# Optimization experiments

Hardware: AMD Instinct MI355X
Metric: run time of the kernel (lower is better)

Reference implementation:

```python
import jax, jax.numpy as jnp
import numpy as np

D_MODEL = 1024
NUM_HEADS = 16
D_K = D_MODEL // NUM_HEADS
THETA = 10000.0


def _apply_rope(x, positions):
    # x: [B, H, S, d_k], positions: [B, S]
    dk = x.shape[-1]
    freq = 1.0 / (THETA ** (jnp.arange(0, dk, 2, dtype=jnp.float32) / dk))  # [dk/2]
    ang = positions.astype(jnp.float32)[:, None, :, None] * freq  # [B,1,S,dk/2]
    cos, sin = jnp.cos(ang), jnp.sin(ang)
    x_even = x[..., 0::2]
    x_odd = x[..., 1::2]
    re = x_even * cos - x_odd * sin
    ro = x_even * sin + x_odd * cos
    # interleave back: [..., dk/2, 2] -> [..., dk]
    return jnp.stack([re, ro], axis=-1).reshape(x.shape)


def setup_inputs() -> dict:
    key = jax.random.key(0)
    kx, kq, kk, kv, ko = jax.random.split(key, 5)
    B, S = 2, 2048
    std = (2.0 / (D_MODEL + D_MODEL)) ** 0.5
    x = jax.random.normal(kx, (B, S, D_MODEL), dtype=jnp.float32)
    Wq = jax.random.normal(kq, (D_MODEL, D_MODEL), dtype=jnp.float32) * std
    Wk = jax.random.normal(kk, (D_MODEL, D_MODEL), dtype=jnp.float32) * std
    Wv = jax.random.normal(kv, (D_MODEL, D_MODEL), dtype=jnp.float32) * std
    Wo = jax.random.normal(ko, (D_MODEL, D_MODEL), dtype=jnp.float32) * std
    token_positions = jnp.tile(jnp.arange(S, dtype=jnp.int32)[None, :], (B, 1))
    return {"x": x, "Wq": Wq, "Wk": Wk, "Wv": Wv, "Wo": Wo,
            "token_positions": token_positions}


def reference(x, Wq, Wk, Wv, Wo, token_positions):
    B, S, D = x.shape
    H, dk = NUM_HEADS, D_K
    scale = 1.0 / np.sqrt(dk)
    # Linear is y = x @ W.T with W:[d_out, d_in]
    q = jnp.einsum('bsd,ed->bse', x, Wq).reshape(B, S, H, dk).transpose(0, 2, 1, 3)
    k = jnp.einsum('bsd,ed->bse', x, Wk).reshape(B, S, H, dk).transpose(0, 2, 1, 3)
    v = jnp.einsum('bsd,ed->bse', x, Wv).reshape(B, S, H, dk).transpose(0, 2, 1, 3)
    q = _apply_rope(q, token_positions)
    k = _apply_rope(k, token_positions)
    scores = jnp.einsum('bhqd,bhkd->bhqk', q, k) * scale  # [B,H,S,S]
    causal = jnp.tril(jnp.ones((S, S), dtype=bool))
    scores = jnp.where(causal[None, None, :, :], scores, -jnp.inf)
    probs = jax.nn.softmax(scores, axis=-1)
    attn = jnp.einsum('bhqk,bhkd->bhqd', probs, v)  # [B,H,S,dk]
    attn = attn.transpose(0, 2, 1, 3).reshape(B, S, D)
    return jnp.einsum('bsd,ed->bse', attn, Wo)
```

## Files before the change

### kernel.cpp

```cpp
#include <hip/hip_runtime.h>
#include <hip/hip_bf16.h>
#include <math.h>

#define B_  2
#define S_  2048
#define H_  16
#define D_  1024
#define DK_ 64

typedef __attribute__((ext_vector_type(8))) short bf16x8;
typedef __attribute__((ext_vector_type(8))) unsigned short ushort8v;
typedef __attribute__((ext_vector_type(4))) float f32x4;

__device__ __forceinline__ unsigned short f2bf(float f) {
  unsigned u = __float_as_uint(f);
  unsigned r = (u + 0x7FFFu + ((u >> 16) & 1u)) >> 16;
  return (unsigned short)r;
}
__device__ __forceinline__ unsigned pack_trunc(float lo, float hi) {
  return (__float_as_uint(lo) >> 16) | (__float_as_uint(hi) & 0xffff0000u);
}
__device__ __forceinline__ float fast_exp2(float x) {
#if __has_builtin(__builtin_amdgcn_exp2f)
  return __builtin_amdgcn_exp2f(x);
#else
  return __expf(x * 0.69314718056f);
#endif
}
__device__ __forceinline__ void gload_lds16(const unsigned short* g,
                                            unsigned short* l) {
  __builtin_amdgcn_global_load_lds(
      (const __attribute__((address_space(1))) unsigned int*)(const void*)g,
      (__attribute__((address_space(3))) unsigned int*)(void*)l, 16, 0, 0);
}

__global__ __launch_bounds__(256)
void cast5_bf16(const float* __restrict__ x,  const float* __restrict__ wq,
                const float* __restrict__ wk, const float* __restrict__ wv,
                const float* __restrict__ wo,
                unsigned short* __restrict__ xb,  unsigned short* __restrict__ wqb,
                unsigned short* __restrict__ wkb, unsigned short* __restrict__ wvb,
                unsigned short* __restrict__ wob)
{
  const int idx = blockIdx.x;
  const float* s; unsigned short* d; int lblk;
  if (idx < 2048) { s = x; d = xb; lblk = idx; }
  else {
    int t = idx - 2048;
    int w = t >> 9;
    lblk  = t & 511;
    s = (w == 0) ? wq  : (w == 1) ? wk  : (w == 2) ? wv  : wo;
    d = (w == 0) ? wqb : (w == 1) ? wkb : (w == 2) ? wvb : wob;
  }
  size_t i0 = ((size_t)lblk * 256 + threadIdx.x) * 8;
  float4 v0 = *(const float4*)(s + i0);
  float4 v1 = *(const float4*)(s + i0 + 4);
  ushort8v o;
  o[0] = f2bf(v0.x); o[1] = f2bf(v0.y); o[2] = f2bf(v0.z); o[3] = f2bf(v0.w);
  o[4] = f2bf(v1.x); o[5] = f2bf(v1.y); o[6] = f2bf(v1.z); o[7] = f2bf(v1.w);
  *(ushort8v*)(d + i0) = o;
}

__global__ __launch_bounds__(256)
void gemm_qkv(const unsigned short* __restrict__ A0,
              const unsigned short* __restrict__ W0,
              const unsigned short* __restrict__ W1,
              const unsigned short* __restrict__ W2,
              unsigned short* __restrict__ qh,
              unsigned short* __restrict__ kh,
              unsigned short* __restrict__ vt,
              const int* __restrict__ tp)
{
  const int z = blockIdx.z;

  __shared__ unsigned short As[128 * 64];
  __shared__ unsigned short Bs[128 * 64];
  __shared__ int tps[128];

  const int tid   = threadIdx.x;
  const int wave  = tid >> 6;
  const int lane  = tid & 63;
  const int quad  = lane >> 4;
  const int col16 = lane & 15;
  const int wr    = (wave >> 1) * 64;
  const int wc    = (wave & 1) * 64;

  const int row0 = (z == 2) ? blockIdx.x * 128 : blockIdx.y * 128;
  const int col0 = (z == 2) ? blockIdx.y * 128 : blockIdx.x * 128;
  const unsigned short* Aptr = (z == 2) ? W2 : A0;
  const unsigned short* Bptr = (z == 0) ? W0 : (z == 1) ? W1 : A0;

  if (z < 2 && tid < 128) tps[tid] = tp[row0 + tid];

  const int srow = wave * 8 + (lane >> 3);
  const int scol = ((lane & 7) ^ ((lane >> 3) & 7)) * 8;
  const unsigned short* gA = Aptr + (size_t)(row0 + srow) * D_ + scol;
  const unsigned short* gB = Bptr + (size_t)(col0 + srow) * D_ + scol;

  f32x4 acc[4][4];
  #pragma unroll
  for (int mt = 0; mt < 4; ++mt)
    #pragma unroll
    for (int nt = 0; nt < 4; ++nt)
      #pragma unroll
      for (int r = 0; r < 4; ++r) acc[mt][nt][r] = 0.f;

  for (int k0 = 0; k0 < D_; k0 += 64) {
    __syncthreads();
    #pragma unroll
    for (int p = 0; p < 4; ++p) {
      gload_lds16(gA + (size_t)(p * 32) * D_ + k0, &As[(p * 32 + wave * 8) * 64]);
      gload_lds16(gB + (size_t)(p * 32) * D_ + k0, &Bs[(p * 32 + wave * 8) * 64]);
    }
    __syncthreads();

    #pragma unroll
    for (int h = 0; h < 2; ++h) {
      const int jo = ((h * 4 + quad) ^ (col16 & 7)) * 8;
      bf16x8 af[4], bfr[4];
      #pragma unroll
      for (int mt = 0; mt < 4; ++mt)
        af[mt] = *(const bf16x8*)&As[(wr + mt * 16 + col16) * 64 + jo];
      #pragma unroll
      for (int nt = 0; nt < 4; ++nt)
        bfr[nt] = *(const bf16x8*)&Bs[(wc + nt * 16 + col16) * 64 + jo];

      #pragma unroll
      for (int mt = 0; mt < 4; ++mt)
        #pragma unroll
        for (int nt = 0; nt < 4; ++nt)
          acc[mt][nt] = __builtin_amdgcn_mfma_f32_16x16x32_bf16(
              af[mt], bfr[nt], acc[mt][nt], 0, 0, 0);
    }
  }

  if (z == 2) {
    #pragma unroll
    for (int mt = 0; mt < 4; ++mt)
      #pragma unroll
      for (int r = 0; r < 4; ++r) {
        int c = row0 + wr + mt * 16 + quad * 4 + r;
        int h = c >> 6, d = c & 63;
        #pragma unroll
        for (int nt = 0; nt < 4; ++nt) {
          int t  = col0 + wc + nt * 16 + col16;
          int bb = t >> 11, sl = t & (S_ - 1);
          vt[((size_t)((bb << 4) + h) * DK_ + d) * S_ + sl] =
              f2bf(acc[mt][nt][r]);
        }
      }
  } else {
    unsigned short* C = z ? kh : qh;
    const float qs = z ? 1.0f : 0.1803368801111204f;
    const float sgn = (col16 & 1) ? 1.f : -1.f;
    float freqr[4];
    #pragma unroll
    for (int nt = 0; nt < 4; ++nt) {
      int i = ((wc + nt * 16 + col16) & 63) >> 1;
      freqr[nt] = exp2f(-0.4152410118f * (float)i);
    }
    #pragma unroll
    for (int mt = 0; mt < 4; ++mt)
      #pragma unroll
      for (int r = 0; r < 4; ++r) {
        int rl  = wr + mt * 16 + quad * 4 + r;
        int row = row0 + rl;
        float p = (float)tps[rl];
        #pragma unroll
        for (int nt = 0; nt < 4; ++nt) {
          int col = col0 + wc + nt * 16 + col16;
          float ang = p * freqr[nt];
          float sn = __sinf(ang), cs = __cosf(ang);
          float val = acc[mt][nt][r];
          float oth = __shfl_xor(val, 1);
          C[(size_t)row * D_ + col] = f2bf((val * cs + oth * sgn * sn) * qs);
        }
      }
  }
}

__global__ __launch_bounds__(256)
void gemm_wo(const unsigned short* __restrict__ A,
             const unsigned short* __restrict__ W,
             float* __restrict__ C)
{
  __shared__ unsigned short As[64 * 64];
  __shared__ unsigned short Bs[128 * 64];

  const int tid   = threadIdx.x;
  const int wave  = tid >> 6;
  const int lane  = tid & 63;
  const int quad  = lane >> 4;
  const int col16 = lane & 15;
  const int row0  = blockIdx.y * 64;
  const int col0  = blockIdx.x * 128;
  const int wr    = (wave >> 1) * 32;
  const int wc    = (wave & 1) * 64;

  const int srow = wave * 8 + (lane >> 3);
  const int scol = ((lane & 7) ^ ((lane >> 3) & 7)) * 8;
  const unsigned short* gA = A + (size_t)(row0 + srow) * D_ + scol;
  const unsigned short* gB = W + (size_t)(col0 + srow) * D_ + scol;

  f32x4 acc[2][4];
  #pragma unroll
  for (int mt = 0; mt < 2; ++mt)
    #pragma unroll
    for (int nt = 0; nt < 4; ++nt)
      #pragma unroll
      for (int r = 0; r < 4; ++r) acc[mt][nt][r] = 0.f;

  for (int k0 = 0; k0 < D_; k0 += 64) {
    __syncthreads();
    #pragma unroll
    for (int p = 0; p < 2; ++p)
      gload_lds16(gA + (size_t)(p * 32) * D_ + k0, &As[(p * 32 + wave * 8) * 64]);
    #pragma unroll
    for (int p = 0; p < 4; ++p)
      gload_lds16(gB + (size_t)(p * 32) * D_ + k0, &Bs[(p * 32 + wave * 8) * 64]);
    __syncthreads();

    #pragma unroll
    for (int h = 0; h < 2; ++h) {
      const int jo = ((h * 4 + quad) ^ (col16 & 7)) * 8;
      bf16x8 af[2], bfr[4];
      #pragma unroll
      for (int mt = 0; mt < 2; ++mt)
        af[mt] = *(const bf16x8*)&As[(wr + mt * 16 + col16) * 64 + jo];
      #pragma unroll
      for (int nt = 0; nt < 4; ++nt)
        bfr[nt] = *(const bf16x8*)&Bs[(wc + nt * 16 + col16) * 64 + jo];

      #pragma unroll
      for (int mt = 0; mt < 2; ++mt)
        #pragma unroll
        for (int nt = 0; nt < 4; ++nt)
          acc[mt][nt] = __builtin_amdgcn_mfma_f32_16x16x32_bf16(
              af[mt], bfr[nt], acc[mt][nt], 0, 0, 0);
    }
  }

  #pragma unroll
  for (int mt = 0; mt < 2; ++mt)
    #pragma unroll
    for (int r = 0; r < 4; ++r) {
      int row = row0 + wr + mt * 16 + quad * 4 + r;
      #pragma unroll
      for (int nt = 0; nt < 4; ++nt) {
        int col = col0 + wc + nt * 16 + col16;
        C[(size_t)row * D_ + col] = acc[mt][nt][r];
      }
    }
}

__device__ __forceinline__ void attn_side(
    const unsigned short* __restrict__ Ks, const unsigned short* __restrict__ Vs,
    unsigned short (* __restrict__ Pl)[72],
    const bf16x8* qf, f32x4* Oacc, float& l_i,
    int quad, int col, int qlocal, bool diag)
{
  const int jx = quad ^ (col & 7);
  f32x4 st[4];
  #pragma unroll
  for (int nb = 0; nb < 4; ++nb) {
    const int s0 = (nb * 16 + col) * 8 + jx;
    bf16x8 ka0 = *(const bf16x8*)(Ks + s0 * 8);
    bf16x8 ka1 = *(const bf16x8*)(Ks + (s0 ^ 4) * 8);
    f32x4 a = {-24.f, -24.f, -24.f, -24.f};
    a = __builtin_amdgcn_mfma_f32_16x16x32_bf16(ka0, qf[0], a, 0, 0, 0);
    a = __builtin_amdgcn_mfma_f32_16x16x32_bf16(ka1, qf[1], a, 0, 0, 0);
    st[nb] = a;
  }

  if (diag) {
    #pragma unroll
    for (int nb = 0; nb < 4; ++nb)
      #pragma unroll
      for (int r = 0; r < 4; ++r)
        if (nb * 16 + quad * 4 + r > qlocal) st[nb][r] = -1e30f;
  }

  float rsum = 0.f;
  #pragma unroll
  for (int nb = 0; nb < 4; ++nb)
    #pragma unroll
    for (int r = 0; r < 4; ++r) {
      float pv = fast_exp2(st[nb][r]);
      st[nb][r] = pv;
      rsum += pv;
    }
  rsum += __shfl_xor(rsum, 16);
  rsum += __shfl_xor(rsum, 32);
  l_i += rsum;

  #pragma unroll
  for (int nb = 0; nb < 4; ++nb) {
    uint2 pk;
    pk.x = pack_trunc(st[nb][0], st[nb][1]);
    pk.y = pack_trunc(st[nb][2], st[nb][3]);
    *(uint2*)&Pl[col][nb * 16 + quad * 4] = pk;
  }

  bf16x8 pf0 = *(const bf16x8*)&Pl[col][quad * 8];
  bf16x8 pf1 = *(const bf16x8*)&Pl[col][32 + quad * 8];
  #pragma unroll
  for (int nb = 0; nb < 4; ++nb) {
    const int s0 = (nb * 16 + col) * 8 + jx;
    bf16x8 va0 = *(const bf16x8*)(Vs + s0 * 8);
    bf16x8 va1 = *(const bf16x8*)(Vs + (s0 ^ 4) * 8);
    Oacc[nb] = __builtin_amdgcn_mfma_f32_16x16x32_bf16(va0, pf0, Oacc[nb], 0, 0, 0);
    Oacc[nb] = __builtin_amdgcn_mfma_f32_16x16x32_bf16(va1, pf1, Oacc[nb], 0, 0, 0);
  }
}

__global__ __launch_bounds__(256)
void attn_mfma(const unsigned short* __restrict__ Q,
               const unsigned short* __restrict__ K,
               const unsigned short* __restrict__ Vt,
               unsigned short* __restrict__ O)
{
  const int qtA  = blockIdx.x;
  const int qtB  = 31 - qtA;
  const int bh   = blockIdx.y;
  const int b    = bh >> 4, h = bh & 15;
  const int tid  = threadIdx.x;
  const int wave = tid >> 6;
  const int lane = tid & 63;
  const int quad = lane >> 4;
  const int col  = lane & 15;
  const int qlocal = wave * 16 + col;

  __shared__ unsigned short Ks[1024 * 8];
  __shared__ unsigned short Vs[1024 * 8];
  __shared__ unsigned short PlA[4][16][72];
  __shared__ unsigned short PlB[4][16][72];

  const size_t qkbase = (size_t)b * S_ * D_ + (size_t)h * DK_;
  const size_t vtbase = (size_t)bh * DK_ * S_;

  const int qrowA = qtA * 64 + qlocal;
  const int qrowB = qtB * 64 + qlocal;
  bf16x8 qfA[2], qfB[2];
  qfA[0] = *(const bf16x8*)(Q + qkbase + (size_t)qrowA * D_ + quad * 8);
  qfA[1] = *(const bf16x8*)(Q + qkbase + (size_t)qrowA * D_ + 32 + quad * 8);
  qfB[0] = *(const bf16x8*)(Q + qkbase + (size_t)qrowB * D_ + quad * 8);
  qfB[1] = *(const bf16x8*)(Q + qkbase + (size_t)qrowB * D_ + 32 + quad * 8);

  const int sr = tid >> 3;
  const int sj = (tid & 7) ^ (sr & 7);
  const unsigned short* gK = K + qkbase + (size_t)sr * D_ + sj * 8;
  const unsigned short* gV = Vt + vtbase + (size_t)sr * S_ + sj * 8;

  f32x4 OaccA[4], OaccB[4];
  #pragma unroll
  for (int nb = 0; nb < 4; ++nb)
    #pragma unroll
    for (int r = 0; r < 4; ++r) { OaccA[nb][r] = 0.f; OaccB[nb][r] = 0.f; }
  float lA = 0.f, lB = 0.f;

  const int nK128 = (qtB + 2) >> 1;

  for (int m = 0; m < nK128; ++m) {
    __syncthreads();
    #pragma unroll
    for (int half = 0; half < 2; ++half) {
      const int kbase = m * 128 + half * 64;
      #pragma unroll
      for (int p = 0; p < 2; ++p) {
        gload_lds16(gK + (size_t)(kbase + p * 32) * D_,
                    &Ks[(size_t)half * 4096 + (size_t)(p * 256 + wave * 64) * 8]);
        gload_lds16(gV + (size_t)(p * 32) * S_ + kbase,
                    &Vs[(size_t)half * 4096 + (size_t)(p * 256 + wave * 64) * 8]);
      }
    }
    __syncthreads();

    #pragma unroll
    for (int half = 0; half < 2; ++half) {
      const int g = 2 * m + half;
      const unsigned short* KsH = Ks + half * 4096;
      const unsigned short* VsH = Vs + half * 4096;
      if (g <= qtB)
        attn_side(KsH, VsH, PlB[wave], qfB, OaccB, lB, quad, col, qlocal,
                  g == qtB);
      if (g <= qtA)
        attn_side(KsH, VsH, PlA[wave], qfA, OaccA, lA, quad, col, qlocal,
                  g == qtA);
    }
  }

  const float invA = 1.0f / lA;
  const float invB = 1.0f / lB;
  #pragma unroll
  for (int nb = 0; nb < 4; ++nb) {
    int d = nb * 16 + quad * 4;
    ushort4 oa, ob;
    oa.x = f2bf(OaccA[nb][0] * invA); oa.y = f2bf(OaccA[nb][1] * invA);
    oa.z = f2bf(OaccA[nb][2] * invA); oa.w = f2bf(OaccA[nb][3] * invA);
    ob.x = f2bf(OaccB[nb][0] * invB); ob.y = f2bf(OaccB[nb][1] * invB);
    ob.z = f2bf(OaccB[nb][2] * invB); ob.w = f2bf(OaccB[nb][3] * invB);
    *(ushort4*)(O + (size_t)b * S_ * D_ + (size_t)qrowA * D_ + h * DK_ + d) = oa;
    *(ushort4*)(O + (size_t)b * S_ * D_ + (size_t)qrowB * D_ + h * DK_ + d) = ob;
  }
}

extern "C" void kernel_launch(void* const* d_in, const int* in_sizes, int n_in,
                              void* d_out, int out_size, void* d_ws, size_t ws_size,
                              hipStream_t stream)
{
  const float* x  = (const float*)d_in[0];
  const float* Wq = (const float*)d_in[1];
  const float* Wk = (const float*)d_in[2];
  const float* Wv = (const float*)d_in[3];
  const float* Wo = (const float*)d_in[4];
  const int*   tp = (const int*)d_in[5];
  float* out = (float*)d_out;

  const size_t NTOK = (size_t)B_ * S_ * D_;
  const size_t NW   = (size_t)D_ * D_;
  unsigned short* qh  = (unsigned short*)d_ws;
  unsigned short* kh  = qh + NTOK;
  unsigned short* vt  = kh + NTOK;
  unsigned short* xb  = vt + NTOK;
  unsigned short* wqb = xb + NTOK;
  unsigned short* wkb = wqb + NW;
  unsigned short* wvb = wkb + NW;
  unsigned short* wob = wvb + NW;
  unsigned short* ab  = xb;

  cast5_bf16<<<dim3(4096), 256, 0, stream>>>(
      x, Wq, Wk, Wv, Wo, xb, wqb, wkb, wvb, wob);

  gemm_qkv<<<dim3(D_ / 128, (B_ * S_) / 128, 3), 256, 0, stream>>>(
      xb, wqb, wkb, wvb, qh, kh, vt, tp);

  attn_mfma<<<dim3(16, B_ * H_), 256, 0, stream>>>(qh, kh, vt, ab);

  gemm_wo<<<dim3(D_ / 128, (B_ * S_) / 64), 256, 0, stream>>>(ab, wob, out);
}
```

Before: 184.7 us.

## Double-buffer attention K/V loads, add MFMA priority hints, swizzle block order

The attention loop now stages 64-key K/V tiles into alternating LDS halves. It prefetches tile g+1 while computing tile g, using explicit vmcnt waits and raw barriers in place of loading 128 keys and then synchronizing. The MFMA sections are raised in wave priority with s_setprio. All three kernels remap block indices into grouped tiles to improve L2 locality of shared operands. The hand-counted vmcnt and barrier scheme adds fragility, and the prefetch overlaps load latency with compute.

New measurement: 180.3 us. 1.02x faster.

```diff
diff --git a/kernel.cpp b/kernel.cpp
--- a/kernel.cpp
+++ b/kernel.cpp
@@ -73,6 +73,10 @@
 {
   const int z = blockIdx.z;
 
+  const int f  = blockIdx.x + (blockIdx.y << 3);
+  const int bx = (f >> 3) & 7;
+  const int by = (f & 7) | ((f >> 6) << 3);
+
   __shared__ unsigned short As[128 * 64];
   __shared__ unsigned short Bs[128 * 64];
   __shared__ int tps[128];
@@ -85,8 +89,8 @@
   const int wr    = (wave >> 1) * 64;
   const int wc    = (wave & 1) * 64;
 
-  const int row0 = (z == 2) ? blockIdx.x * 128 : blockIdx.y * 128;
-  const int col0 = (z == 2) ? blockIdx.y * 128 : blockIdx.x * 128;
+  const int row0 = (z == 2) ? bx * 128 : by * 128;
+  const int col0 = (z == 2) ? by * 128 : bx * 128;
   const unsigned short* Aptr = (z == 2) ? W2 : A0;
   const unsigned short* Bptr = (z == 0) ? W0 : (z == 1) ? W1 : A0;
 
@@ -187,13 +191,17 @@
   __shared__ unsigned short As[64 * 64];
   __shared__ unsigned short Bs[128 * 64];
 
+  const int f  = blockIdx.x + (blockIdx.y << 3);
+  const int bx = (f >> 3) & 7;
+  const int by = (f & 7) | ((f >> 6) << 3);
+
   const int tid   = threadIdx.x;
   const int wave  = tid >> 6;
   const int lane  = tid & 63;
   const int quad  = lane >> 4;
   const int col16 = lane & 15;
-  const int row0  = blockIdx.y * 64;
-  const int col0  = blockIdx.x * 128;
+  const int row0  = by * 64;
+  const int col0  = bx * 128;
   const int wr    = (wave >> 1) * 32;
   const int wc    = (wave & 1) * 64;
 
@@ -261,6 +269,7 @@
 {
   const int jx = quad ^ (col & 7);
   f32x4 st[4];
+  __builtin_amdgcn_s_setprio(1);
   #pragma unroll
   for (int nb = 0; nb < 4; ++nb) {
     const int s0 = (nb * 16 + col) * 8 + jx;
@@ -271,6 +280,7 @@
     a = __builtin_amdgcn_mfma_f32_16x16x32_bf16(ka1, qf[1], a, 0, 0, 0);
     st[nb] = a;
   }
+  __builtin_amdgcn_s_setprio(0);
 
   if (diag) {
     #pragma unroll
@@ -303,6 +313,7 @@
 
   bf16x8 pf0 = *(const bf16x8*)&Pl[col][quad * 8];
   bf16x8 pf1 = *(const bf16x8*)&Pl[col][32 + quad * 8];
+  __builtin_amdgcn_s_setprio(1);
   #pragma unroll
   for (int nb = 0; nb < 4; ++nb) {
     const int s0 = (nb * 16 + col) * 8 + jx;
@@ -311,6 +322,7 @@
     Oacc[nb] = __builtin_amdgcn_mfma_f32_16x16x32_bf16(va0, pf0, Oacc[nb], 0, 0, 0);
     Oacc[nb] = __builtin_amdgcn_mfma_f32_16x16x32_bf16(va1, pf1, Oacc[nb], 0, 0, 0);
   }
+  __builtin_amdgcn_s_setprio(0);
 }
 
 __global__ __launch_bounds__(256)
@@ -319,9 +331,10 @@
                const unsigned short* __restrict__ Vt,
                unsigned short* __restrict__ O)
 {
-  const int qtA  = blockIdx.x;
+  const int f    = blockIdx.x + (blockIdx.y << 4);
+  const int qtA  = (f >> 3) & 15;
+  const int bh   = (f & 7) | ((f >> 7) << 3);
   const int qtB  = 31 - qtA;
-  const int bh   = blockIdx.y;
   const int b    = bh >> 4, h = bh & 15;
   const int tid  = threadIdx.x;
   const int wave = tid >> 6;
@@ -358,35 +371,41 @@
     for (int r = 0; r < 4; ++r) { OaccA[nb][r] = 0.f; OaccB[nb][r] = 0.f; }
   float lA = 0.f, lB = 0.f;
 
-  const int nK128 = (qtB + 2) >> 1;
-
-  for (int m = 0; m < nK128; ++m) {
-    __syncthreads();
-    #pragma unroll
-    for (int half = 0; half < 2; ++half) {
-      const int kbase = m * 128 + half * 64;
-      #pragma unroll
-      for (int p = 0; p < 2; ++p) {
-        gload_lds16(gK + (size_t)(kbase + p * 32) * D_,
-                    &Ks[(size_t)half * 4096 + (size_t)(p * 256 + wave * 64) * 8]);
-        gload_lds16(gV + (size_t)(p * 32) * S_ + kbase,
-                    &Vs[(size_t)half * 4096 + (size_t)(p * 256 + wave * 64) * 8]);
-      }
-    }
-    __syncthreads();
-
-    #pragma unroll
-    for (int half = 0; half < 2; ++half) {
-      const int g = 2 * m + half;
-      const unsigned short* KsH = Ks + half * 4096;
-      const unsigned short* VsH = Vs + half * 4096;
-      if (g <= qtB)
-        attn_side(KsH, VsH, PlB[wave], qfB, OaccB, lB, quad, col, qlocal,
-                  g == qtB);
-      if (g <= qtA)
-        attn_side(KsH, VsH, PlA[wave], qfA, OaccA, lA, quad, col, qlocal,
-                  g == qtA);
-    }
+  const int nH = qtB + 1;
+
+  auto stage = [&](int g) {
+    const int kbase = g << 6;
+    unsigned short* Kd = Ks + (g & 1) * 4096 + wave * 512;
+    unsigned short* Vd = Vs + (g & 1) * 4096 + wave * 512;
+    #pragma unroll
+    for (int p = 0; p < 2; ++p) {
+      gload_lds16(gK + (size_t)(kbase + p * 32) * D_, Kd + p * 2048);
+      gload_lds16(gV + (size_t)(p * 32) * S_ + kbase, Vd + p * 2048);
+    }
+  };
+
+  stage(0);
+
+  for (int g = 0; g < nH; ++g) {
+    if (g + 1 < nH) {
+      stage(g + 1);
+      asm volatile("s_waitcnt vmcnt(4)" ::: "memory");
+    } else {
+      asm volatile("s_waitcnt vmcnt(0)" ::: "memory");
+    }
+    __builtin_amdgcn_s_barrier();
+    __builtin_amdgcn_sched_barrier(0);
+
+    const unsigned short* KsH = Ks + (g & 1) * 4096;
+    const unsigned short* VsH = Vs + (g & 1) * 4096;
+    attn_side(KsH, VsH, PlB[wave], qfB, OaccB, lB, quad, col, qlocal,
+              g == qtB);
+    if (g <= qtA)
+      attn_side(KsH, VsH, PlA[wave], qfA, OaccA, lA, quad, col, qlocal,
+                g == qtA);
+
+    __builtin_amdgcn_sched_barrier(0);
+    __builtin_amdgcn_s_barrier();
   }
 
   const float invA = 1.0f / lA;
```
